# Kernel tuning notes

Measured on AMD Instinct MI355X. Metric: run time of the kernel, lower is better.

## Reference

```python
import jax, jax.numpy as jnp
import numpy as np

B, S, D = 4, 2048, 1024
H = 16
HD = D // H  # 64
MASKED_BIAS = jnp.float32(-10000.0)


def setup_inputs() -> dict:
    key = jax.random.key(0)
    ks = jax.random.split(key, 5)
    std = 0.02
    return {
        "hidden_states": jax.random.normal(ks[0], (B, S, D), jnp.float32),
        "Wq": jax.random.normal(ks[1], (D, D), jnp.float32) * std,
        "bq": jnp.zeros((D,), jnp.float32),
        "Wk": jax.random.normal(ks[2], (D, D), jnp.float32) * std,
        "bk": jnp.zeros((D,), jnp.float32),
        "Wv": jax.random.normal(ks[3], (D, D), jnp.float32) * std,
        "bv": jnp.zeros((D,), jnp.float32),
        "Wo": jax.random.normal(ks[4], (D, D), jnp.float32) * std,
        "bo": jnp.zeros((D,), jnp.float32),
    }


def _split_heads(x):
    # [B, S, D] -> [B, H, S, HD]
    return x.reshape(B, S, H, HD).transpose(0, 2, 1, 3)


def reference(hidden_states, Wq, bq, Wk, bk, Wv, bv, Wo, bo):
    q = _split_heads(hidden_states @ Wq + bq)
    k = _split_heads(hidden_states @ Wk + bk)
    v = _split_heads(hidden_states @ Wv + bv)

    # scores [B, H, S, S], scaled by sqrt(head_dim) (scale=True)
    w = jnp.einsum("bhqd,bhkd->bhqk", q, k) / jnp.sqrt(jnp.float32(HD))
    causal = jnp.tril(jnp.ones((S, S), dtype=bool))  # [S, S]
    w = jnp.where(causal[None, None], w, MASKED_BIAS)
    w = jax.nn.softmax(w, axis=-1)
    # attn_pdrop = 0.0 -> dropout is identity

    a = jnp.einsum("bhqk,bhkd->bhqd", w, v)  # [B, H, S, HD]
    a = a.transpose(0, 2, 1, 3).reshape(B, S, D)  # merge heads
    out = a @ Wo + bo
    # resid_pdrop = 0.0 -> identity
    return out
```

## Files before the change

kernel.cpp:

```cpp
#include <hip/hip_runtime.h>
#include <stdint.h>

typedef unsigned short u16;
typedef __bf16 bf16x2 __attribute__((ext_vector_type(2)));
typedef __bf16 bf16x8 __attribute__((ext_vector_type(8)));
typedef float f32x4 __attribute__((ext_vector_type(4)));
typedef float f32x16 __attribute__((ext_vector_type(16)));
typedef unsigned int u32x4 __attribute__((ext_vector_type(4)));
typedef u16 u16x8 __attribute__((ext_vector_type(8)));
typedef u16 u16x4 __attribute__((ext_vector_type(4)));

#define MFMA16(a, b, c) __builtin_amdgcn_mfma_f32_16x16x32_bf16((a), (b), (c), 0, 0, 0)
#define MFMA32(a, b, c) __builtin_amdgcn_mfma_f32_32x32x16_bf16((a), (b), (c), 0, 0, 0)

#define QSCALE 0.18033688011112042f

#if defined(__has_builtin)
#if __has_builtin(__builtin_amdgcn_exp2f)
#define EXP2(x) __builtin_amdgcn_exp2f(x)
#endif
#endif
#ifndef EXP2
#define EXP2(x) __expf((x) * 0.6931471805599453f)
#endif

__device__ __forceinline__ u16 f2bf(float f) {
  return __builtin_bit_cast(u16, (__bf16)f);
}

__device__ __forceinline__ unsigned cvtpk(float lo, float hi) {
  bf16x2 t;
  t[0] = (__bf16)lo;
  t[1] = (__bf16)hi;
  return __builtin_bit_cast(unsigned, t);
}

__device__ __forceinline__ bf16x8 load_frag(const u16* lds_base, int byteoff) {
  u32x4 v = *(const u32x4*)((const char*)lds_base + byteoff);
  return __builtin_bit_cast(bf16x8, v);
}

#define GLOAD_LDS16(gp, lp)                                                        \
  __builtin_amdgcn_global_load_lds((const __attribute__((address_space(1))) void*)(gp), \
                                   (__attribute__((address_space(3))) void*)(lp), 16, 0, 0)

template <int ROWS>
__device__ __forceinline__ void stage_tile(const u16* __restrict__ src, int ld, u16* lds,
                                           int tid) {
  constexpr int SLOTS = ROWS * 8;
#pragma unroll
  for (int it = 0; it < SLOTS / 256; ++it) {
    const int s = it * 256 + tid;
    const int row = s >> 3;
    const int seg = (s & 7) ^ (row & 7);
    const u16* g = src + row * ld + seg * 8;
    u16* l = lds + (it * 256 + (tid & ~63)) * 8;
    GLOAD_LDS16(g, l);
  }
}


__global__ __launch_bounds__(256) void cvt_x(const float* __restrict__ in,
                                             u16* __restrict__ out) {
  const int i = (int)blockIdx.x * 256 + (int)threadIdx.x;
  const float4 a = ((const float4*)in)[2 * i];
  const float4 b = ((const float4*)in)[2 * i + 1];
  u16x8 o;
  o[0] = f2bf(a.x); o[1] = f2bf(a.y); o[2] = f2bf(a.z); o[3] = f2bf(a.w);
  o[4] = f2bf(b.x); o[5] = f2bf(b.y); o[6] = f2bf(b.z); o[7] = f2bf(b.w);
  ((u16x8*)out)[i] = o;
}

__global__ __launch_bounds__(256) void cvt_w_t(const float* __restrict__ W,
                                               u16* __restrict__ Wt) {
  __shared__ u16 t[64][65];
  const int tid = (int)threadIdx.x;
  const int r = tid >> 2;
  const int cs = (tid & 3) * 16;
  const int tr = (int)blockIdx.y * 64;
  const int tc = (int)blockIdx.x * 64;
#pragma unroll
  for (int i = 0; i < 16; i += 4) {
    const float4 v = *(const float4*)&W[(size_t)(tr + r) * 1024 + tc + cs + i];
    t[r][cs + i + 0] = f2bf(v.x);
    t[r][cs + i + 1] = f2bf(v.y);
    t[r][cs + i + 2] = f2bf(v.z);
    t[r][cs + i + 3] = f2bf(v.w);
  }
  __syncthreads();
  u16 tmp[16];
#pragma unroll
  for (int i = 0; i < 16; ++i) tmp[i] = t[cs + i][r];
  u16x8 o0, o1;
#pragma unroll
  for (int i = 0; i < 8; ++i) { o0[i] = tmp[i]; o1[i] = tmp[8 + i]; }
  *(u16x8*)&Wt[(size_t)(tc + r) * 1024 + tr + cs] = o0;
  *(u16x8*)&Wt[(size_t)(tc + r) * 1024 + tr + cs + 8] = o1;
}


template <int OUT_MODE>
__global__ __launch_bounds__(256) void gemm_bt(const u16* __restrict__ A,
                                               const u16* __restrict__ Bt,
                                               const float* __restrict__ bias,
                                               void* __restrict__ Cout) {
  constexpr int N = 1024, K = 1024;
  __shared__ __align__(16) u16 lds[2 * 128 * 64];
  const int tid = (int)threadIdx.x;
  const int w = tid >> 6, lane = tid & 63;
  const int wm = w >> 1, wn = w & 1;
  const int lr = lane & 15, lg = lane >> 4;
  const int mt = (int)blockIdx.y, nt = (int)blockIdx.x;

  const u16* Abase = A + (size_t)mt * 128 * K;
  const u16* Bbase = Bt + (size_t)nt * 128 * K;

  f32x4 acc[4][4] = {};

  for (int k0 = 0; k0 < K; k0 += 64) {
    stage_tile<128>(Abase + k0, K, lds, tid);
    stage_tile<128>(Bbase + k0, K, lds + 128 * 64, tid);
    __syncthreads();
#pragma unroll
    for (int ks = 0; ks < 2; ++ks) {
      bf16x8 af[4], bf[4];
#pragma unroll
      for (int i = 0; i < 4; ++i) {
        const int ar = wm * 64 + i * 16 + lr;
        af[i] = load_frag(lds, ar * 128 + ((ks * 64 + lg * 16) ^ ((ar & 7) << 4)));
        const int br = wn * 64 + i * 16 + lr;
        bf[i] = load_frag(lds + 128 * 64, br * 128 + ((ks * 64 + lg * 16) ^ ((br & 7) << 4)));
      }
#pragma unroll
      for (int mf = 0; mf < 4; ++mf)
#pragma unroll
        for (int nf = 0; nf < 4; ++nf) acc[mf][nf] = MFMA16(af[mf], bf[nf], acc[mf][nf]);
    }
    __syncthreads();
  }

#pragma unroll
  for (int mf = 0; mf < 4; ++mf) {
#pragma unroll
    for (int nf = 0; nf < 4; ++nf) {
      const int col = nt * 128 + wn * 64 + nf * 16 + lr;
      const float bv = bias[col];
#pragma unroll
      for (int r = 0; r < 4; ++r) {
        const int row = mt * 128 + wm * 64 + mf * 16 + lg * 4 + r;
        const float v = acc[mf][nf][r] + bv;
        if (OUT_MODE == 0) {
          ((u16*)Cout)[(size_t)row * N + col] = f2bf(v * QSCALE);
        } else if (OUT_MODE == 1) {
          ((float*)Cout)[(size_t)row * N + col] = v;
        } else if (OUT_MODE == 2) {
          const int b = row >> 11, s = row & 2047;
          const int h = col >> 6, d = col & 63;
          const size_t addr = ((size_t)((b * 16 + h) * 32 + (s >> 6))) * 4096 +
                              (size_t)(d >> 5) * 2048 + (size_t)((s & 63) >> 4) * 512 +
                              (size_t)((d & 31) | (((s >> 3) & 1) << 5)) * 8 + (s & 7);
          ((u16*)Cout)[addr] = f2bf(v);
        } else {
          const int b = row >> 11, s = row & 2047;
          const int h = col >> 6, d = col & 63;
          const size_t addr = ((size_t)((b * 16 + h) * 64 + (s >> 5))) * 2048 +
                              (size_t)(d >> 4) * 512 +
                              (size_t)((s & 31) | (((d >> 3) & 1) << 5)) * 8 + (d & 7);
          ((u16*)Cout)[addr] = f2bf(v);
        }
      }
    }
  }
}


__device__ __forceinline__ void loadK(bf16x8 (&kf)[2][4], const u16* __restrict__ p) {
#pragma unroll
  for (int sb = 0; sb < 2; ++sb)
#pragma unroll
    for (int dk = 0; dk < 4; ++dk)
      kf[sb][dk] = *(const bf16x8*)(p + sb * 2048 + dk * 512);
}

__device__ __forceinline__ void attn_tile(const bf16x8 (&kf)[2][4],
                                          const u16* __restrict__ vp_tile,
                                          const bf16x8 (&qf)[4], const int hi,
                                          const bool masked, const int tmask, f32x16& o0,
                                          f32x16& o1, float& m_run, float& l_run) {
  bf16x8 vf[2][4];
#pragma unroll
  for (int db = 0; db < 2; ++db)
#pragma unroll
    for (int ks = 0; ks < 4; ++ks)
      vf[db][ks] = *(const bf16x8*)(vp_tile + db * 2048 + ks * 512);

  f32x16 p0 = {}, p1 = {};
#pragma unroll
  for (int dk = 0; dk < 4; ++dk) {
    p0 = MFMA32(kf[0][dk], qf[dk], p0);
    p1 = MFMA32(kf[1][dk], qf[dk], p1);
  }

  if (masked) {
#pragma unroll
    for (int r = 0; r < 16; ++r) {
      const int kl = (r & 3) + 8 * (r >> 2) + 4 * hi;
      if (kl > tmask) p0[r] = -1.0e30f;
      if (kl + 32 > tmask) p1[r] = -1.0e30f;
    }
  }

  float mx = -3.0e38f;
#pragma unroll
  for (int r = 0; r < 16; ++r) mx = fmaxf(mx, fmaxf(p0[r], p1[r]));
  mx = fmaxf(mx, __shfl_xor(mx, 32));

  if (__any(mx > m_run + 11.5416f)) {
    const float mnew = fmaxf(m_run, mx);
    const float alpha = EXP2(m_run - mnew);
    m_run = mnew;
    l_run *= alpha;
#pragma unroll
    for (int r = 0; r < 16; ++r) { o0[r] *= alpha; o1[r] *= alpha; }
  }

  float rs = 0.0f;
#pragma unroll
  for (int r = 0; r < 16; ++r) {
    p0[r] = EXP2(p0[r] - m_run);
    p1[r] = EXP2(p1[r] - m_run);
    rs += p0[r] + p1[r];
  }
  rs += __shfl_xor(rs, 32);
  l_run += rs;

  unsigned c[16];
#pragma unroll
  for (int j = 0; j < 8; ++j) {
    c[j] = cvtpk(p0[2 * j], p0[2 * j + 1]);
    c[8 + j] = cvtpk(p1[2 * j], p1[2 * j + 1]);
  }
  bf16x8 pf[4];
#pragma unroll
  for (int ks = 0; ks < 4; ++ks) {
    const int base = (ks >> 1) * 8 + (ks & 1) * 4;
    auto s0 = __builtin_amdgcn_permlane32_swap(c[base + 0], c[base + 2], false, false);
    auto s1 = __builtin_amdgcn_permlane32_swap(c[base + 1], c[base + 3], false, false);
    u32x4 wv;
    wv[0] = s0[0];
    wv[1] = s1[0];
    wv[2] = s0[1];
    wv[3] = s1[1];
    pf[ks] = __builtin_bit_cast(bf16x8, wv);
  }

#pragma unroll
  for (int ks = 0; ks < 4; ++ks) {
    o0 = MFMA32(vf[0][ks], pf[ks], o0);
    o1 = MFMA32(vf[1][ks], pf[ks], o1);
  }
}

__global__ __launch_bounds__(64) void attn_fwd(const u16* __restrict__ Qb,
                                               const u16* __restrict__ Kf,
                                               const u16* __restrict__ Vf,
                                               u16* __restrict__ Ab) {
  const int lane = (int)threadIdx.x;
  const int ln = lane & 31, hi = lane >> 5;

  const int id = (int)blockIdx.x;
  const int xcd = id & 7, r = id >> 3;
  const int bh = (xcd << 3) | (r & 7);
  const int qs = 63 - (r >> 3);
  const int b = bh >> 4, h = bh & 15;
  const int wq = qs * 32;
  const int qrow = wq + ln;

  const u16* qp = Qb + (size_t)(b * 2048 + qrow) * 1024 + h * 64 + hi * 8;
  bf16x8 qf[4];
#pragma unroll
  for (int dk = 0; dk < 4; ++dk) qf[dk] = *(const bf16x8*)(qp + dk * 16);

  const u16* kp = Kf + (size_t)bh * 131072 + lane * 8;
  const u16* vp = Vf + (size_t)bh * 131072 + lane * 8;

  f32x16 o0 = {}, o1 = {};
  float m_run = -3.0e38f, l_run = 0.0f;

  const int nt = (qs >> 1) + 1;
  bf16x8 kA[2][4], kB[2][4];
  loadK(kA, kp);
  int i = 0;
  while (i + 2 <= nt) {
    loadK(kB, kp + (size_t)(i + 1) * 4096);
    attn_tile(kA, vp + (size_t)i * 4096, qf, hi, false, 0, o0, o1, m_run, l_run);
    const int nx = (i + 2 < nt) ? i + 2 : i + 1;
    loadK(kA, kp + (size_t)nx * 4096);
    attn_tile(kB, vp + (size_t)(i + 1) * 4096, qf, hi, i + 2 == nt, qrow - (i + 1) * 64,
              o0, o1, m_run, l_run);
    i += 2;
  }
  if (i < nt)
    attn_tile(kA, vp + (size_t)i * 4096, qf, hi, true, qrow - i * 64, o0, o1, m_run, l_run);

  const float inv = 1.0f / l_run;
  u16* op = Ab + (size_t)(b * 2048 + qrow) * 1024 + h * 64;
#pragma unroll
  for (int rr = 0; rr < 4; ++rr) {
    u16x4 s0v, s1v;
#pragma unroll
    for (int cc = 0; cc < 4; ++cc) {
      s0v[cc] = f2bf(o0[rr * 4 + cc] * inv);
      s1v[cc] = f2bf(o1[rr * 4 + cc] * inv);
    }
    *(u16x4*)(op + rr * 8 + hi * 4) = s0v;
    *(u16x4*)(op + 32 + rr * 8 + hi * 4) = s1v;
  }
}


extern "C" void kernel_launch(void* const* d_in, const int* in_sizes, int n_in, void* d_out,
                              int out_size, void* d_ws, size_t ws_size, hipStream_t stream) {
  const float* X = (const float*)d_in[0];
  const float* Wq = (const float*)d_in[1];
  const float* bq = (const float*)d_in[2];
  const float* Wk = (const float*)d_in[3];
  const float* bk = (const float*)d_in[4];
  const float* Wv = (const float*)d_in[5];
  const float* bv = (const float*)d_in[6];
  const float* Wo = (const float*)d_in[7];
  const float* bo = (const float*)d_in[8];
  float* out = (float*)d_out;

  u16* ws = (u16*)d_ws;
  u16* Xb = ws;
  u16* Wqt = Xb + 8388608;
  u16* Wkt = Wqt + 1048576;
  u16* Wvt = Wkt + 1048576;
  u16* Wot = Wvt + 1048576;
  u16* Qb = Wot + 1048576;
  u16* Kf = Qb + 8388608;
  u16* Vf = Kf + 8388608;
  u16* Ab = Vf + 8388608;

  cvt_x<<<4096, 256, 0, stream>>>(X, Xb);
  dim3 wtg(16, 16);
  cvt_w_t<<<wtg, 256, 0, stream>>>(Wq, Wqt);
  cvt_w_t<<<wtg, 256, 0, stream>>>(Wk, Wkt);
  cvt_w_t<<<wtg, 256, 0, stream>>>(Wv, Wvt);
  cvt_w_t<<<wtg, 256, 0, stream>>>(Wo, Wot);

  dim3 gg(8, 64);
  gemm_bt<0><<<gg, 256, 0, stream>>>(Xb, Wqt, bq, Qb);
  gemm_bt<3><<<gg, 256, 0, stream>>>(Xb, Wkt, bk, Kf);
  gemm_bt<2><<<gg, 256, 0, stream>>>(Xb, Wvt, bv, Vf);

  attn_fwd<<<4096, 64, 0, stream>>>(Qb, Kf, Vf, Ab);

  gemm_bt<1><<<gg, 256, 0, stream>>>(Ab, Wot, bo, out);
}
```

Before: 182.9 us.

## Fuse QKV projections into one launch and pack four balanced query tiles per attention block

The three separate Q/K/V GEMM launches become one gemm_qkv launch with a 24x64 grid, where blockIdx.x selects the weight matrix and output layout. The attention kernel moves from 64-thread single-wave blocks to 256-thread blocks of four waves. Each block pairs query tiles slot, 31-slot, 32+slot and 63-slot so causal work is balanced across the block. This is meant to cut launch overhead and tail imbalance and to improve occupancy, but it adds a runtime branch on the output mode in the QKV epilogue.

```diff
diff --git a/kernel.cpp b/kernel.cpp
--- a/kernel.cpp
+++ b/kernel.cpp
@@ -99,12 +99,103 @@
 }
 
 
-template <int OUT_MODE>
-__global__ __launch_bounds__(256) void gemm_bt(const u16* __restrict__ A,
-                                               const u16* __restrict__ Bt,
-                                               const float* __restrict__ bias,
-                                               void* __restrict__ Cout) {
-  constexpr int N = 1024, K = 1024;
+__device__ __forceinline__ size_t vfrag_addr(int row, int col) {
+  const int b = row >> 11, s = row & 2047;
+  const int h = col >> 6, d = col & 63;
+  return ((size_t)((b * 16 + h) * 32 + (s >> 6))) * 4096 + (size_t)(d >> 5) * 2048 +
+         (size_t)((s & 63) >> 4) * 512 + (size_t)((d & 31) | (((s >> 3) & 1) << 5)) * 8 +
+         (s & 7);
+}
+
+__device__ __forceinline__ size_t kfrag_addr(int row, int col) {
+  const int b = row >> 11, s = row & 2047;
+  const int h = col >> 6, d = col & 63;
+  return ((size_t)((b * 16 + h) * 64 + (s >> 5))) * 2048 + (size_t)(d >> 4) * 512 +
+         (size_t)((s & 31) | (((d >> 3) & 1) << 5)) * 8 + (d & 7);
+}
+
+
+__device__ __forceinline__ void gemm_core(const u16* __restrict__ Abase,
+                                          const u16* __restrict__ Bbase, u16* lds, int tid,
+                                          int wm, int wn, int lr, int lg,
+                                          f32x4 (&acc)[4][4]) {
+  constexpr int K = 1024;
+  for (int k0 = 0; k0 < K; k0 += 64) {
+    stage_tile<128>(Abase + k0, K, lds, tid);
+    stage_tile<128>(Bbase + k0, K, lds + 128 * 64, tid);
+    __syncthreads();
+#pragma unroll
+    for (int ks = 0; ks < 2; ++ks) {
+      bf16x8 af[4], bf[4];
+#pragma unroll
+      for (int i = 0; i < 4; ++i) {
+        const int ar = wm * 64 + i * 16 + lr;
+        af[i] = load_frag(lds, ar * 128 + ((ks * 64 + lg * 16) ^ ((ar & 7) << 4)));
+        const int br = wn * 64 + i * 16 + lr;
+        bf[i] = load_frag(lds + 128 * 64, br * 128 + ((ks * 64 + lg * 16) ^ ((br & 7) << 4)));
+      }
+#pragma unroll
+      for (int mf = 0; mf < 4; ++mf)
+#pragma unroll
+        for (int nf = 0; nf < 4; ++nf) acc[mf][nf] = MFMA16(af[mf], bf[nf], acc[mf][nf]);
+    }
+    __syncthreads();
+  }
+}
+
+
+__global__ __launch_bounds__(256) void gemm_qkv(const u16* __restrict__ A,
+                                                const u16* __restrict__ Bq,
+                                                const u16* __restrict__ Bk,
+                                                const u16* __restrict__ Bv,
+                                                const float* __restrict__ bq,
+                                                const float* __restrict__ bk,
+                                                const float* __restrict__ bv,
+                                                u16* __restrict__ Qo, u16* __restrict__ Ko,
+                                                u16* __restrict__ Vo) {
+  __shared__ __align__(16) u16 lds[2 * 128 * 64];
+  const int tid = (int)threadIdx.x;
+  const int w = tid >> 6, lane = tid & 63;
+  const int wm = w >> 1, wn = w & 1;
+  const int lr = lane & 15, lg = lane >> 4;
+  const int g = (int)blockIdx.x;
+  const int m_idx = g >> 3, nt = g & 7;
+  const int mt = (int)blockIdx.y;
+
+  const u16* Bt = m_idx == 0 ? Bq : (m_idx == 1 ? Bk : Bv);
+  const float* bias = m_idx == 0 ? bq : (m_idx == 1 ? bk : bv);
+
+  f32x4 acc[4][4] = {};
+  gemm_core(A + (size_t)mt * 128 * 1024, Bt + (size_t)nt * 128 * 1024, lds, tid, wm, wn, lr,
+            lg, acc);
+
+#pragma unroll
+  for (int mf = 0; mf < 4; ++mf) {
+#pragma unroll
+    for (int nf = 0; nf < 4; ++nf) {
+      const int col = nt * 128 + wn * 64 + nf * 16 + lr;
+      const float bv2 = bias[col];
+#pragma unroll
+      for (int r = 0; r < 4; ++r) {
+        const int row = mt * 128 + wm * 64 + mf * 16 + lg * 4 + r;
+        const float v = acc[mf][nf][r] + bv2;
+        if (m_idx == 0) {
+          Qo[(size_t)row * 1024 + col] = f2bf(v * QSCALE);
+        } else if (m_idx == 1) {
+          Ko[kfrag_addr(row, col)] = f2bf(v);
+        } else {
+          Vo[vfrag_addr(row, col)] = f2bf(v);
+        }
+      }
+    }
+  }
+}
+
+
+__global__ __launch_bounds__(256) void gemm_out(const u16* __restrict__ A,
+                                                const u16* __restrict__ Bt,
+                                                const float* __restrict__ bias,
+                                                float* __restrict__ Cout) {
   __shared__ __align__(16) u16 lds[2 * 128 * 64];
   const int tid = (int)threadIdx.x;
   const int w = tid >> 6, lane = tid & 63;
@@ -112,32 +203,9 @@
   const int lr = lane & 15, lg = lane >> 4;
   const int mt = (int)blockIdx.y, nt = (int)blockIdx.x;
 
-  const u16* Abase = A + (size_t)mt * 128 * K;
-  const u16* Bbase = Bt + (size_t)nt * 128 * K;
-
   f32x4 acc[4][4] = {};
-
-  for (int k0 = 0; k0 < K; k0 += 64) {
-    stage_tile<128>(Abase + k0, K, lds, tid);
-    stage_tile<128>(Bbase + k0, K, lds + 128 * 64, tid);
-    __syncthreads();
-#pragma unroll
-    for (int ks = 0; ks < 2; ++ks) {
-      bf16x8 af[4], bf[4];
-#pragma unroll
-      for (int i = 0; i < 4; ++i) {
-        const int ar = wm * 64 + i * 16 + lr;
-        af[i] = load_frag(lds, ar * 128 + ((ks * 64 + lg * 16) ^ ((ar & 7) << 4)));
-        const int br = wn * 64 + i * 16 + lr;
-        bf[i] = load_frag(lds + 128 * 64, br * 128 + ((ks * 64 + lg * 16) ^ ((br & 7) << 4)));
-      }
-#pragma unroll
-      for (int mf = 0; mf < 4; ++mf)
-#pragma unroll
-        for (int nf = 0; nf < 4; ++nf) acc[mf][nf] = MFMA16(af[mf], bf[nf], acc[mf][nf]);
-    }
-    __syncthreads();
-  }
+  gemm_core(A + (size_t)mt * 128 * 1024, Bt + (size_t)nt * 128 * 1024, lds, tid, wm, wn, lr,
+            lg, acc);
 
 #pragma unroll
   for (int mf = 0; mf < 4; ++mf) {
@@ -148,26 +216,7 @@
 #pragma unroll
       for (int r = 0; r < 4; ++r) {
         const int row = mt * 128 + wm * 64 + mf * 16 + lg * 4 + r;
-        const float v = acc[mf][nf][r] + bv;
-        if (OUT_MODE == 0) {
-          ((u16*)Cout)[(size_t)row * N + col] = f2bf(v * QSCALE);
-        } else if (OUT_MODE == 1) {
-          ((float*)Cout)[(size_t)row * N + col] = v;
-        } else if (OUT_MODE == 2) {
-          const int b = row >> 11, s = row & 2047;
-          const int h = col >> 6, d = col & 63;
-          const size_t addr = ((size_t)((b * 16 + h) * 32 + (s >> 6))) * 4096 +
-                              (size_t)(d >> 5) * 2048 + (size_t)((s & 63) >> 4) * 512 +
-                              (size_t)((d & 31) | (((s >> 3) & 1) << 5)) * 8 + (s & 7);
-          ((u16*)Cout)[addr] = f2bf(v);
-        } else {
-          const int b = row >> 11, s = row & 2047;
-          const int h = col >> 6, d = col & 63;
-          const size_t addr = ((size_t)((b * 16 + h) * 64 + (s >> 5))) * 2048 +
-                              (size_t)(d >> 4) * 512 +
-                              (size_t)((s & 31) | (((d >> 3) & 1) << 5)) * 8 + (d & 7);
-          ((u16*)Cout)[addr] = f2bf(v);
-        }
+        Cout[(size_t)row * 1024 + col] = acc[mf][nf][r] + bv;
       }
     }
   }
@@ -261,17 +310,19 @@
   }
 }
 
-__global__ __launch_bounds__(64) void attn_fwd(const u16* __restrict__ Qb,
-                                               const u16* __restrict__ Kf,
-                                               const u16* __restrict__ Vf,
-                                               u16* __restrict__ Ab) {
-  const int lane = (int)threadIdx.x;
+__global__ __launch_bounds__(256) void attn_fwd(const u16* __restrict__ Qb,
+                                                const u16* __restrict__ Kf,
+                                                const u16* __restrict__ Vf,
+                                                u16* __restrict__ Ab) {
+  const int tid = (int)threadIdx.x;
+  const int w = tid >> 6, lane = tid & 63;
   const int ln = lane & 31, hi = lane >> 5;
 
   const int id = (int)blockIdx.x;
-  const int xcd = id & 7, r = id >> 3;
-  const int bh = (xcd << 3) | (r & 7);
-  const int qs = 63 - (r >> 3);
+  const int xcd = id & 7;
+  const int bh = (xcd << 3) | ((id >> 3) & 7);
+  const int slot = id >> 6;
+  const int qs = (w == 0) ? slot : (w == 1) ? 31 - slot : (w == 2) ? 32 + slot : 63 - slot;
   const int b = bh >> 4, h = bh & 15;
   const int wq = qs * 32;
   const int qrow = wq + ln;
@@ -350,12 +401,11 @@
   cvt_w_t<<<wtg, 256, 0, stream>>>(Wv, Wvt);
   cvt_w_t<<<wtg, 256, 0, stream>>>(Wo, Wot);
 
+  dim3 qkvg(24, 64);
+  gemm_qkv<<<qkvg, 256, 0, stream>>>(Xb, Wqt, Wkt, Wvt, bq, bk, bv, Qb, Kf, Vf);
+
+  attn_fwd<<<1024, 256, 0, stream>>>(Qb, Kf, Vf, Ab);
+
   dim3 gg(8, 64);
-  gemm_bt<0><<<gg, 256, 0, stream>>>(Xb, Wqt, bq, Qb);
-  gemm_bt<3><<<gg, 256, 0, stream>>>(Xb, Wkt, bk, Kf);
-  gemm_bt<2><<<gg, 256, 0, stream>>>(Xb, Wvt, bv, Vf);
-
-  attn_fwd<<<4096, 64, 0, stream>>>(Qb, Kf, Vf, Ab);
-
-  gemm_bt<1><<<gg, 256, 0, stream>>>(Ab, Wot, bo, out);
-}
+  gemm_out<<<gg, 256, 0, stream>>>(Ab, Wot, bo, out);
+}
```

Result: slower. 220.7 us (+20.7%).
